# Kernel optimization log

Measured on AMD Instinct MI355X. Metric: run time of the kernel, lower is better.

The kernel has to match this reference:

```python
import jax, jax.numpy as jnp
import numpy as np


def setup_inputs() -> dict:
    key = jax.random.key(0)
    kq, kk, kv = jax.random.split(key, 3)
    B, S, D = 16, 4096, 64
    q = jax.random.normal(kq, (B, S, D), dtype=jnp.float32)
    k = jax.random.normal(kk, (B, S, D), dtype=jnp.float32)
    v = jax.random.normal(kv, (B, S, D), dtype=jnp.float32)
    return {"q": q, "k": k, "v": v}


def reference(q, k, v):
    # scale = 1/sqrt(head_dim), the canonical value passed as `scale` in the repo
    scale = 1.0 / jnp.sqrt(jnp.asarray(q.shape[-1], dtype=q.dtype))
    # scores: [B, Sq, Sk] = q @ k^T  (torch.bmm(q, k.transpose(1,2)))
    scores = jnp.einsum("bqd,bkd->bqk", q, k) * scale
    # softmax over key dim (dim=2); dropout p=0.0 is identity in eval
    attention = jax.nn.softmax(scores, axis=2)
    # context: [B, Sq, D] = attention @ v
    context = jnp.einsum("bqk,bkd->bqd", attention, v)
    return (context, attention)
```

## Files before the change

kernel.cpp:

```cpp
#include <hip/hip_runtime.h>
#include <stdint.h>

typedef _Float16 f16x8 __attribute__((ext_vector_type(8)));
typedef _Float16 f16x4 __attribute__((ext_vector_type(4)));
typedef float    f32x4 __attribute__((ext_vector_type(4)));

#define S_LEN 4096
#define D_DIM 64
#define NB 16
constexpr size_t NE = (size_t)NB * S_LEN * D_DIM;

__global__ __launch_bounds__(256) void k_prep3(const float* __restrict__ k,
                                               _Float16* __restrict__ k3) {
  int g = blockIdx.x * 256 + threadIdx.x;
  int tile = g >> 9, c = g & 511;
  int grp = c >> 6, lane = c & 63;
  int ds = grp >> 2, nf = grp & 3;
  int row = nf * 16 + (lane & 15);
  int d0 = ds * 32 + ((lane >> 4) << 3);
  const float* src = k + ((size_t)tile * 64 + row) * D_DIM + d0;
  f32x4 a = *reinterpret_cast<const f32x4*>(src);
  f32x4 b4 = *reinterpret_cast<const f32x4*>(src + 4);
  f16x8 o;
#pragma unroll
  for (int i = 0; i < 4; ++i) {
    o[i] = (_Float16)a[i];
    o[i + 4] = (_Float16)b4[i];
  }
  *reinterpret_cast<f16x8*>(k3 + (size_t)g * 8) = o;
}

__global__ __launch_bounds__(256) void v_prep3(const float* __restrict__ v,
                                               _Float16* __restrict__ v3) {
  __shared__ float t[64][65];
  int tile = blockIdx.x;
  int c = threadIdx.x & 63, rg = threadIdx.x >> 6;
#pragma unroll
  for (int j = 0; j < 16; ++j)
    t[rg + 4 * j][c] = v[((size_t)tile * 64 + rg + 4 * j) * D_DIM + c];
  __syncthreads();
  _Float16* dst = v3 + (size_t)tile * 4096;
#pragma unroll
  for (int j = 0; j < 4; ++j) {
    int cc = threadIdx.x + 256 * j;
    int g = cc >> 6, lane = cc & 63;
    int nf = g >> 2, dn = g & 3;
    int kl = nf * 16 + ((lane >> 4) << 2);
    int d = dn * 16 + (lane & 15);
    f16x4 o;
#pragma unroll
    for (int i = 0; i < 4; ++i) o[i] = (_Float16)t[kl + i][d];
    *reinterpret_cast<f16x4*>(dst + ((g >> 1) << 9) + lane * 8 + ((g & 1) << 2)) = o;
  }
}

constexpr float CEXP = 0.18033688011112042f;

#define PIPE_BARRIER()                                 \
  do {                                                 \
    asm volatile("s_waitcnt lgkmcnt(0)" ::: "memory"); \
    __builtin_amdgcn_s_barrier();                      \
    __builtin_amdgcn_sched_barrier(0);                 \
  } while (0)

__global__ __launch_bounds__(256, 4) void attn_k(const float* __restrict__ q,
                                                 const _Float16* __restrict__ k3,
                                                 const _Float16* __restrict__ v3,
                                                 float* __restrict__ ctx,
                                                 float* __restrict__ att) {
  __shared__ _Float16 ktile[4][4096];
  const int tid = threadIdx.x, w = tid >> 6, lane = tid & 63;
  const int l15 = lane & 15, lh = lane >> 4;
  const int bid = blockIdx.x;
  const int logical = (bid & 7) * 128 + (bid >> 3);
  const int b = logical >> 6, qt = logical & 63;
  const int qrow = qt * 64 + w * 16 + l15;

  f16x8 qf[2];
#pragma unroll
  for (int ds = 0; ds < 2; ++ds) {
    const float* qp = q + ((size_t)b * S_LEN + qrow) * D_DIM + ds * 32 + 8 * lh;
    f32x4 a = *reinterpret_cast<const f32x4*>(qp);
    f32x4 c4 = *reinterpret_cast<const f32x4*>(qp + 4);
#pragma unroll
    for (int i = 0; i < 4; ++i) {
      qf[ds][i] = (_Float16)a[i];
      qf[ds][i + 4] = (_Float16)c4[i];
    }
  }

  const _Float16* k3b = k3 + (size_t)(b * 64) * 4096;

  f16x8 s0, s1, s2, s3;
  auto load2 = [&](int ta, int tb) {
    const _Float16* sa_ = k3b + (size_t)ta * 4096;
    const _Float16* sb_ = k3b + (size_t)tb * 4096;
    s0 = *reinterpret_cast<const f16x8*>(sa_ + tid * 8);
    s1 = *reinterpret_cast<const f16x8*>(sa_ + (tid + 256) * 8);
    s2 = *reinterpret_cast<const f16x8*>(sb_ + tid * 8);
    s3 = *reinterpret_cast<const f16x8*>(sb_ + (tid + 256) * 8);
  };
  auto write2 = [&](int set) {
    *reinterpret_cast<f16x8*>(&ktile[set * 2][tid * 8]) = s0;
    *reinterpret_cast<f16x8*>(&ktile[set * 2][(tid + 256) * 8]) = s1;
    *reinterpret_cast<f16x8*>(&ktile[set * 2 + 1][tid * 8]) = s2;
    *reinterpret_cast<f16x8*>(&ktile[set * 2 + 1][(tid + 256) * 8]) = s3;
  };

  auto qk = [&](int buf, f32x4(&sa)[4]) {
#pragma unroll
    for (int ds = 0; ds < 2; ++ds)
#pragma unroll
      for (int nf = 0; nf < 4; ++nf) {
        const int g = ds * 4 + nf;
        f16x8 kf = *reinterpret_cast<const f16x8*>(&ktile[buf][(g * 64 + lane) * 8]);
        sa[nf] = __builtin_amdgcn_mfma_f32_16x16x32_f16(kf, qf[ds], sa[nf], 0, 0, 0);
      }
  };

  load2(0, 1);
  write2(0);
  PIPE_BARRIER();
  load2(2, 3);
  float ls[4] = {};
  for (int p = 0; p < 32; ++p) {
    const int set = p & 1;
    write2(set ^ 1);
    const int na = 2 * p + 4 < 64 ? 2 * p + 4 : 62;
    load2(na, na + 1);
#pragma unroll
    for (int half = 0; half < 2; ++half) {
      f32x4 sa[4] = {};
      __builtin_amdgcn_s_setprio(1);
      qk(set * 2 + half, sa);
      __builtin_amdgcn_s_setprio(0);
#pragma unroll
      for (int nf = 0; nf < 4; ++nf)
#pragma unroll
        for (int r = 0; r < 4; ++r) ls[nf] += exp2f(sa[nf][r] * CEXP);
    }
    PIPE_BARRIER();
  }
  float lsum = (ls[0] + ls[1]) + (ls[2] + ls[3]);
  lsum += __shfl_xor(lsum, 16);
  lsum += __shfl_xor(lsum, 32);
  const float lb = -__log2f(lsum);

  load2(0, 1);
  write2(0);
  PIPE_BARRIER();
  load2(2, 3);
  f32x4 ca[4] = {};
  float* attrow = att + ((size_t)b * S_LEN + qrow) * S_LEN;
  const _Float16* v3b = v3 + (size_t)(b * 64) * 4096 + lane * 8;
  for (int p = 0; p < 32; ++p) {
    const int set = p & 1;
    write2(set ^ 1);
    const int na = 2 * p + 4 < 64 ? 2 * p + 4 : 62;
    load2(na, na + 1);
#pragma unroll
    for (int half = 0; half < 2; ++half) {
      const int t = 2 * p + half;
      const _Float16* vp = v3b + (size_t)t * 4096;
      f16x8 vv8[8];
#pragma unroll
      for (int g2 = 0; g2 < 8; ++g2)
        vv8[g2] = *reinterpret_cast<const f16x8*>(vp + (size_t)g2 * 512);
      f32x4 sa[4] = {};
      __builtin_amdgcn_s_setprio(1);
      qk(set * 2 + half, sa);
      __builtin_amdgcn_s_setprio(0);
      f16x4 pb[4];
#pragma unroll
      for (int nf = 0; nf < 4; ++nf) {
        f32x4 pf;
        pf[0] = exp2f(sa[nf][0] * CEXP + lb);
        pf[1] = exp2f(sa[nf][1] * CEXP + lb);
        pf[2] = exp2f(sa[nf][2] * CEXP + lb);
        pf[3] = exp2f(sa[nf][3] * CEXP + lb);
        *reinterpret_cast<f32x4*>(attrow + t * 64 + nf * 16 + 4 * lh) = pf;
        pb[nf][0] = (_Float16)pf[0];
        pb[nf][1] = (_Float16)pf[1];
        pb[nf][2] = (_Float16)pf[2];
        pb[nf][3] = (_Float16)pf[3];
      }
      __builtin_amdgcn_s_setprio(1);
#pragma unroll
      for (int nf = 0; nf < 4; ++nf)
#pragma unroll
        for (int dn = 0; dn < 4; ++dn) {
          const int g = nf * 4 + dn;
          f16x4 vf = (g & 1) ? __builtin_shufflevector(vv8[g >> 1], vv8[g >> 1], 4, 5, 6, 7)
                             : __builtin_shufflevector(vv8[g >> 1], vv8[g >> 1], 0, 1, 2, 3);
          ca[dn] = __builtin_amdgcn_mfma_f32_16x16x16f16(vf, pb[nf], ca[dn], 0, 0, 0);
        }
      __builtin_amdgcn_s_setprio(0);
    }
    PIPE_BARRIER();
  }
#pragma unroll
  for (int dn = 0; dn < 4; ++dn)
    *reinterpret_cast<f32x4*>(ctx + ((size_t)b * S_LEN + qrow) * D_DIM + dn * 16 + 4 * lh) =
        ca[dn];
}

extern "C" void kernel_launch(void* const* d_in, const int* in_sizes, int n_in,
                              void* d_out, int out_size, void* d_ws, size_t ws_size,
                              hipStream_t stream) {
  const float* q = (const float*)d_in[0];
  const float* k = (const float*)d_in[1];
  const float* v = (const float*)d_in[2];
  float* ctx = (float*)d_out;
  float* att = ctx + NE;

  _Float16* k3 = (_Float16*)d_ws;
  _Float16* v3 = (_Float16*)((char*)d_ws + 2 * NE);

  k_prep3<<<(int)(NE / 8 / 256), 256, 0, stream>>>(k, k3);
  v_prep3<<<NB * 64, 256, 0, stream>>>(v, v3);
  attn_k<<<1024, 256, 0, stream>>>(q, k3, v3, ctx, att);
}
```

Measured before the change: 405.7 us.

## Split softmax-denominator pass across waves by key range, loading K directly to registers

The first pass, which computes the row sums of exp(scores), is restructured. Each wave now handles a quarter of the key tiles for all 64 query rows of the block, loading K fragments straight from global memory into registers with double buffering and no LDS staging or barriers. Each K fragment is reused across two query row groups per MFMA pair. Partial sums are reduced across waves through a small shared array. This removes the LDS writes and barriers of the first pass, at the cost of more registers and uncoalesced-per-wave global K reads.

```diff
diff --git a/kernel.cpp b/kernel.cpp
--- a/kernel.cpp
+++ b/kernel.cpp
@@ -69,13 +69,81 @@
                                                  float* __restrict__ ctx,
                                                  float* __restrict__ att) {
   __shared__ _Float16 ktile[4][4096];
+  __shared__ float red[4][4][16];
   const int tid = threadIdx.x, w = tid >> 6, lane = tid & 63;
   const int l15 = lane & 15, lh = lane >> 4;
   const int bid = blockIdx.x;
   const int logical = (bid & 7) * 128 + (bid >> 3);
   const int b = logical >> 6, qt = logical & 63;
+
+  const _Float16* k3b = k3 + (size_t)(b * 64) * 4096;
+
+  {
+    const _Float16* kt0 = k3b + lane * 8;
+    float pls[4] = {0.f, 0.f, 0.f, 0.f};
+#pragma unroll
+    for (int pr = 0; pr < 2; ++pr) {
+      f16x8 qp2[2][2];
+#pragma unroll
+      for (int j = 0; j < 2; ++j) {
+        const int qrow = qt * 64 + (2 * pr + j) * 16 + l15;
+#pragma unroll
+        for (int ds = 0; ds < 2; ++ds) {
+          const float* qp = q + ((size_t)b * S_LEN + qrow) * D_DIM + ds * 32 + 8 * lh;
+          f32x4 a = *reinterpret_cast<const f32x4*>(qp);
+          f32x4 c4 = *reinterpret_cast<const f32x4*>(qp + 4);
+#pragma unroll
+          for (int i = 0; i < 4; ++i) {
+            qp2[j][ds][i] = (_Float16)a[i];
+            qp2[j][ds][i + 4] = (_Float16)c4[i];
+          }
+        }
+      }
+      f16x8 ka[8], kb[8];
+      auto loadk = [&](int t, f16x8(&kf)[8]) {
+        const _Float16* p = kt0 + (size_t)t * 4096;
+#pragma unroll
+        for (int g = 0; g < 8; ++g) kf[g] = *reinterpret_cast<const f16x8*>(p + g * 512);
+      };
+      auto comp2 = [&](const f16x8(&kf8)[8]) {
+        f32x4 sa2[2][4] = {};
+#pragma unroll
+        for (int ds = 0; ds < 2; ++ds)
+#pragma unroll
+          for (int nf = 0; nf < 4; ++nf) {
+            f16x8 kf = kf8[ds * 4 + nf];
+            sa2[0][nf] = __builtin_amdgcn_mfma_f32_16x16x32_f16(kf, qp2[0][ds], sa2[0][nf], 0, 0, 0);
+            sa2[1][nf] = __builtin_amdgcn_mfma_f32_16x16x32_f16(kf, qp2[1][ds], sa2[1][nf], 0, 0, 0);
+          }
+#pragma unroll
+        for (int j = 0; j < 2; ++j)
+#pragma unroll
+          for (int nf = 0; nf < 4; ++nf)
+#pragma unroll
+            for (int r = 0; r < 4; ++r)
+              pls[2 * pr + j] += exp2f(sa2[j][nf][r] * CEXP);
+      };
+      const int tb = w * 16;
+      loadk(tb, ka);
+      for (int t2 = 0; t2 < 16; t2 += 2) {
+        loadk(tb + t2 + 1, kb);
+        comp2(ka);
+        if (t2 + 2 < 16) loadk(tb + t2 + 2, ka);
+        comp2(kb);
+      }
+    }
+#pragma unroll
+    for (int f = 0; f < 4; ++f) {
+      pls[f] += __shfl_xor(pls[f], 16);
+      pls[f] += __shfl_xor(pls[f], 32);
+      if (lh == 0) red[w][f][l15] = pls[f];
+    }
+  }
+  __syncthreads();
+  const float lb =
+      -__log2f(red[0][w][l15] + red[1][w][l15] + red[2][w][l15] + red[3][w][l15]);
+
   const int qrow = qt * 64 + w * 16 + l15;
-
   f16x8 qf[2];
 #pragma unroll
   for (int ds = 0; ds < 2; ++ds) {
@@ -89,12 +157,10 @@
     }
   }
 
-  const _Float16* k3b = k3 + (size_t)(b * 64) * 4096;
-
   f16x8 s0, s1, s2, s3;
-  auto load2 = [&](int ta, int tb) {
+  auto load2 = [&](int ta, int tb2) {
     const _Float16* sa_ = k3b + (size_t)ta * 4096;
-    const _Float16* sb_ = k3b + (size_t)tb * 4096;
+    const _Float16* sb_ = k3b + (size_t)tb2 * 4096;
     s0 = *reinterpret_cast<const f16x8*>(sa_ + tid * 8);
     s1 = *reinterpret_cast<const f16x8*>(sa_ + (tid + 256) * 8);
     s2 = *reinterpret_cast<const f16x8*>(sb_ + tid * 8);
@@ -117,34 +183,6 @@
         sa[nf] = __builtin_amdgcn_mfma_f32_16x16x32_f16(kf, qf[ds], sa[nf], 0, 0, 0);
       }
   };
-
-  load2(0, 1);
-  write2(0);
-  PIPE_BARRIER();
-  load2(2, 3);
-  float ls[4] = {};
-  for (int p = 0; p < 32; ++p) {
-    const int set = p & 1;
-    write2(set ^ 1);
-    const int na = 2 * p + 4 < 64 ? 2 * p + 4 : 62;
-    load2(na, na + 1);
-#pragma unroll
-    for (int half = 0; half < 2; ++half) {
-      f32x4 sa[4] = {};
-      __builtin_amdgcn_s_setprio(1);
-      qk(set * 2 + half, sa);
-      __builtin_amdgcn_s_setprio(0);
-#pragma unroll
-      for (int nf = 0; nf < 4; ++nf)
-#pragma unroll
-        for (int r = 0; r < 4; ++r) ls[nf] += exp2f(sa[nf][r] * CEXP);
-    }
-    PIPE_BARRIER();
-  }
-  float lsum = (ls[0] + ls[1]) + (ls[2] + ls[3]);
-  lsum += __shfl_xor(lsum, 16);
-  lsum += __shfl_xor(lsum, 32);
-  const float lb = -__log2f(lsum);
 
   load2(0, 1);
   write2(0);
```

Measured after the change: 458.4 us. 1.13x slower.

## Fuse row-sum pass with PV accumulation and fold scale into Q

Applied to the files above, without the earlier changes.

The softmax scale is folded into the Q fragments at load time, so exponentials no longer need a per-element multiply. The separate first pass that only computed row sums is merged into the PV pass: unnormalized exponentials feed the PV MFMA and the row sum, and the context is divided by the sum at the end. A final pass recomputes QK with the log-sum offset to write the normalized attention matrix. The V loads and PV MFMAs now run alongside the sum accumulation instead of the attention stores, and unnormalized values are rounded to fp16 without a max subtraction, which could overflow for large scores.

```diff
diff --git a/kernel.cpp b/kernel.cpp
--- a/kernel.cpp
+++ b/kernel.cpp
@@ -84,17 +84,17 @@
     f32x4 c4 = *reinterpret_cast<const f32x4*>(qp + 4);
 #pragma unroll
     for (int i = 0; i < 4; ++i) {
-      qf[ds][i] = (_Float16)a[i];
-      qf[ds][i + 4] = (_Float16)c4[i];
+      qf[ds][i] = (_Float16)(a[i] * CEXP);
+      qf[ds][i + 4] = (_Float16)(c4[i] * CEXP);
     }
   }
 
   const _Float16* k3b = k3 + (size_t)(b * 64) * 4096;
 
   f16x8 s0, s1, s2, s3;
-  auto load2 = [&](int ta, int tb) {
+  auto load2 = [&](int ta, int tb2) {
     const _Float16* sa_ = k3b + (size_t)ta * 4096;
-    const _Float16* sb_ = k3b + (size_t)tb * 4096;
+    const _Float16* sb_ = k3b + (size_t)tb2 * 4096;
     s0 = *reinterpret_cast<const f16x8*>(sa_ + tid * 8);
     s1 = *reinterpret_cast<const f16x8*>(sa_ + (tid + 256) * 8);
     s2 = *reinterpret_cast<const f16x8*>(sb_ + tid * 8);
@@ -118,41 +118,14 @@
       }
   };
 
+  const _Float16* v3b = v3 + (size_t)(b * 64) * 4096 + lane * 8;
+
   load2(0, 1);
   write2(0);
   PIPE_BARRIER();
   load2(2, 3);
   float ls[4] = {};
-  for (int p = 0; p < 32; ++p) {
-    const int set = p & 1;
-    write2(set ^ 1);
-    const int na = 2 * p + 4 < 64 ? 2 * p + 4 : 62;
-    load2(na, na + 1);
-#pragma unroll
-    for (int half = 0; half < 2; ++half) {
-      f32x4 sa[4] = {};
-      __builtin_amdgcn_s_setprio(1);
-      qk(set * 2 + half, sa);
-      __builtin_amdgcn_s_setprio(0);
-#pragma unroll
-      for (int nf = 0; nf < 4; ++nf)
-#pragma unroll
-        for (int r = 0; r < 4; ++r) ls[nf] += exp2f(sa[nf][r] * CEXP);
-    }
-    PIPE_BARRIER();
-  }
-  float lsum = (ls[0] + ls[1]) + (ls[2] + ls[3]);
-  lsum += __shfl_xor(lsum, 16);
-  lsum += __shfl_xor(lsum, 32);
-  const float lb = -__log2f(lsum);
-
-  load2(0, 1);
-  write2(0);
-  PIPE_BARRIER();
-  load2(2, 3);
   f32x4 ca[4] = {};
-  float* attrow = att + ((size_t)b * S_LEN + qrow) * S_LEN;
-  const _Float16* v3b = v3 + (size_t)(b * 64) * 4096 + lane * 8;
   for (int p = 0; p < 32; ++p) {
     const int set = p & 1;
     write2(set ^ 1);
@@ -174,11 +147,11 @@
 #pragma unroll
       for (int nf = 0; nf < 4; ++nf) {
         f32x4 pf;
-        pf[0] = exp2f(sa[nf][0] * CEXP + lb);
-        pf[1] = exp2f(sa[nf][1] * CEXP + lb);
-        pf[2] = exp2f(sa[nf][2] * CEXP + lb);
-        pf[3] = exp2f(sa[nf][3] * CEXP + lb);
-        *reinterpret_cast<f32x4*>(attrow + t * 64 + nf * 16 + 4 * lh) = pf;
+        pf[0] = exp2f(sa[nf][0]);
+        pf[1] = exp2f(sa[nf][1]);
+        pf[2] = exp2f(sa[nf][2]);
+        pf[3] = exp2f(sa[nf][3]);
+        ls[nf] += (pf[0] + pf[1]) + (pf[2] + pf[3]);
         pb[nf][0] = (_Float16)pf[0];
         pb[nf][1] = (_Float16)pf[1];
         pb[nf][2] = (_Float16)pf[2];
@@ -198,10 +171,48 @@
     }
     PIPE_BARRIER();
   }
-#pragma unroll
-  for (int dn = 0; dn < 4; ++dn)
-    *reinterpret_cast<f32x4*>(ctx + ((size_t)b * S_LEN + qrow) * D_DIM + dn * 16 + 4 * lh) =
-        ca[dn];
+  float lsum = (ls[0] + ls[1]) + (ls[2] + ls[3]);
+  lsum += __shfl_xor(lsum, 16);
+  lsum += __shfl_xor(lsum, 32);
+  const float linv = 1.0f / lsum;
+  const float lb = -__log2f(lsum);
+
+#pragma unroll
+  for (int dn = 0; dn < 4; ++dn) {
+    f32x4 co = ca[dn];
+    co[0] *= linv; co[1] *= linv; co[2] *= linv; co[3] *= linv;
+    *reinterpret_cast<f32x4*>(ctx + ((size_t)b * S_LEN + qrow) * D_DIM + dn * 16 + 4 * lh) = co;
+  }
+
+  load2(0, 1);
+  write2(0);
+  PIPE_BARRIER();
+  load2(2, 3);
+  float* attrow = att + ((size_t)b * S_LEN + qrow) * S_LEN;
+  for (int p = 0; p < 32; ++p) {
+    const int set = p & 1;
+    write2(set ^ 1);
+    const int na = 2 * p + 4 < 64 ? 2 * p + 4 : 62;
+    load2(na, na + 1);
+#pragma unroll
+    for (int half = 0; half < 2; ++half) {
+      const int t = 2 * p + half;
+      f32x4 sa[4] = {};
+      __builtin_amdgcn_s_setprio(1);
+      qk(set * 2 + half, sa);
+      __builtin_amdgcn_s_setprio(0);
+#pragma unroll
+      for (int nf = 0; nf < 4; ++nf) {
+        f32x4 pf;
+        pf[0] = exp2f(sa[nf][0] + lb);
+        pf[1] = exp2f(sa[nf][1] + lb);
+        pf[2] = exp2f(sa[nf][2] + lb);
+        pf[3] = exp2f(sa[nf][3] + lb);
+        *reinterpret_cast<f32x4*>(attrow + t * 64 + nf * 16 + 4 * lh) = pf;
+      }
+    }
+    PIPE_BARRIER();
+  }
 }
 
 extern "C" void kernel_launch(void* const* d_in, const int* in_sizes, int n_in,
```

Result: no change. 397.9 us (median of 3 runs) (-1.9%).
